# Kernel tuning notes

Hardware: AMD Instinct MI355X
Metric: run time of the kernel (lower is better)

The kernel has to match this reference:

```python
import jax, jax.numpy as jnp
import numpy as np

G, N, E, D, K = 32, 512, 8192, 256, 2048
LAMB_EDGE = 1.0
LAMB_NODE = 0.0
CODEBOOK_WEIGHT = 1000.0
ALPHA = 100.0


def setup_inputs() -> dict:
    key = jax.random.key(0)
    ks = jax.random.split(key, 12)
    s = 1.0 / np.sqrt(D)
    return {
        'feats': jax.random.normal(ks[0], (G, N, D), jnp.float32),
        'src': jax.random.randint(ks[1], (G, E), 0, N, jnp.int32),
        'dst': jax.random.randint(ks[2], (G, E), 0, N, jnp.int32),
        'W1': jax.random.normal(ks[3], (D, D), jnp.float32) * s,
        'b1': jnp.zeros((D,), jnp.float32),
        'W2': jax.random.normal(ks[4], (D, D), jnp.float32) * s,
        'b2': jnp.zeros((D,), jnp.float32),
        'ln_gamma': jnp.ones((D,), jnp.float32),
        'ln_beta': jnp.zeros((D,), jnp.float32),
        'dec1_W': jax.random.normal(ks[5], (D, D), jnp.float32) * s,
        'dec1_b': jnp.zeros((D,), jnp.float32),
        'dec2_W': jax.random.normal(ks[6], (D, D), jnp.float32) * s,
        'dec2_b': jnp.zeros((D,), jnp.float32),
        'codebook': jax.random.normal(ks[7], (K, D), jnp.float32),
    }


def _graph_conv(x, src, dst, W, b):
    # DGL GraphConv, norm='both': D_out^{-1/2} -> sum aggregate -> D_in^{-1/2} -> linear -> relu
    ones_e = jnp.ones(src.shape[0], x.dtype)
    deg_out = jnp.clip(jax.ops.segment_sum(ones_e, src, num_segments=N), 1.0)
    deg_in = jnp.clip(jax.ops.segment_sum(ones_e, dst, num_segments=N), 1.0)
    h = x * jax.lax.rsqrt(deg_out)[:, None]
    m = jax.ops.segment_sum(h[src], dst, num_segments=N)
    m = m * jax.lax.rsqrt(deg_in)[:, None]
    return jax.nn.relu(m @ W + b)


def _layernorm(x, gamma, beta):
    mu = jnp.mean(x, axis=-1, keepdims=True)
    var = jnp.mean(jnp.square(x - mu), axis=-1, keepdims=True)
    return (x - mu) * jax.lax.rsqrt(var + 1e-5) * gamma + beta


def _edge_loss(qe, src, dst):
    # qe: [N, D] decoded node embeddings for one graph
    logits = qe @ qe.T  # [N, N]
    adj = jnp.zeros((N, N), qe.dtype).at[src, dst].set(1.0)
    mask = jnp.triu(jnp.ones((N, N), bool), k=1)
    num_possible = N * N / 2.0
    num_edges = jnp.sum(jnp.where(mask, adj, 0.0))
    pos_weight = (num_possible - num_edges) / (num_edges + 1e-6)
    # BCEWithLogits with pos_weight, mean over strict upper triangle
    per = pos_weight * adj * jax.nn.softplus(-logits) + (1.0 - adj) * jax.nn.softplus(logits)
    return jnp.sum(jnp.where(mask, per, 0.0)) / (N * (N - 1) / 2.0)


def reference(feats, src, dst, W1, b1, W2, b2, ln_gamma, ln_beta,
              dec1_W, dec1_b, dec2_W, dec2_b, codebook):
    conv = jax.vmap(_graph_conv, in_axes=(0, 0, 0, None, None))
    h1 = conv(feats, src, dst, W1, b1)              # [G, N, D]
    h1 = _layernorm(h1, ln_gamma, ln_beta)           # dropout eval = identity
    h2 = conv(h1, src, dst, W2, b2)                  # [G, N, D]

    hf = h2.reshape(G * N, D)
    # cosine-sim VQ
    xn = hf * jax.lax.rsqrt(jnp.sum(hf * hf, -1, keepdims=True) + 1e-12)
    cn = codebook * jax.lax.rsqrt(jnp.sum(codebook * codebook, -1, keepdims=True) + 1e-12)
    dist = xn @ cn.T                                 # [G*N, K] cosine similarities
    idx = jnp.argmax(dist, axis=-1)
    q = codebook[idx]
    q_st = hf + jax.lax.stop_gradient(q - hf)        # straight-through
    vq_loss = CODEBOOK_WEIGHT * jnp.mean(jnp.square(q - jax.lax.stop_gradient(hf)))

    quantized_edge = (q_st @ dec1_W + dec1_b).reshape(G, N, D)
    quantized_node = q_st @ dec2_W + dec2_b

    edge_losses = jax.vmap(_edge_loss)(quantized_edge, src, dst)  # [G]
    edge_rec_loss = LAMB_EDGE * jnp.mean(edge_losses)
    feature_rec_loss = LAMB_NODE * jnp.mean(jnp.square(hf - quantized_node))
    loss = feature_rec_loss + edge_rec_loss * ALPHA + vq_loss
    return loss
```

## Files before the change

### kernel.cpp

```cpp
#include <hip/hip_runtime.h>
#include <math.h>

#define G 32
#define N 512
#define E 8192
#define D 256
#define KCB 2048
#define GN (G * N)

typedef __bf16 bf16x8 __attribute__((ext_vector_type(8)));
typedef float f32x4 __attribute__((ext_vector_type(4)));

static const size_t OFF_SPOS   = 0;
static const size_t OFF_SNEG   = OFF_SPOS + 256;
static const size_t OFF_BEST   = OFF_SNEG + 256;
static const size_t ZERO_BYTES = OFF_BEST + (size_t)GN * 8;
static const size_t OFF_NEDGE  = ZERO_BYTES;
static const size_t OFF_VQPART = OFF_NEDGE + 256;
static const size_t OFF_ROWOFF = OFF_VQPART + (size_t)GN * 4;
static const size_t OFF_RS_OUT = OFF_ROWOFF + (size_t)GN * 4;
static const size_t OFF_RS_IN  = OFF_RS_OUT + (size_t)GN * 4;
static const size_t OFF_DEG_IN = OFF_RS_IN + (size_t)GN * 4;
static const size_t OFF_CSR    = OFF_DEG_IN + (size_t)GN * 4;
static const size_t OFF_ADJ    = OFF_CSR + (size_t)G * E * 4;
static const size_t OFF_RNC    = OFF_ADJ + (size_t)G * N * N / 8;
static const size_t OFF_W1T    = OFF_RNC + (size_t)KCB * 4;
static const size_t OFF_W2T    = OFF_W1T + (size_t)D * D * 2;
static const size_t OFF_DWT    = OFF_W2T + (size_t)D * D * 2;
static const size_t OFF_CBB    = OFF_DWT + (size_t)D * D * 2;
static const size_t OFF_FEB    = OFF_CBB + (size_t)KCB * D * 2;
static const size_t OFF_AGGB   = OFF_FEB + (size_t)GN * D * 2;
static const size_t OFF_BF32   = OFF_AGGB + (size_t)GN * D * 2;
static const size_t OFF_BCB    = OFF_BF32 + (size_t)GN * D * 4;

__global__ void __launch_bounds__(512) k_graph_build(
    const int* __restrict__ src, const int* __restrict__ dst,
    unsigned* __restrict__ adj, int* __restrict__ nedge, int* __restrict__ row_off_g,
    float* __restrict__ rs_in_g, float* __restrict__ rs_out_g,
    int* __restrict__ deg_in_g, int* __restrict__ csr_src) {
  int g = blockIdx.x, t = threadIdx.x;
  __shared__ unsigned s_adj[N * N / 32];
  __shared__ int s_deg_in[N], s_deg_out[N];
  __shared__ int s_buf[2][N];
  __shared__ int s_red[8];
  for (int i = t; i < N * N / 32; i += 512) s_adj[i] = 0;
  s_deg_in[t] = 0;
  s_deg_out[t] = 0;
  __syncthreads();
  const int* sg = src + g * E;
  const int* dg = dst + g * E;
  int se[E / 512], de[E / 512];
  int ecount = 0;
#pragma unroll
  for (int j = 0; j < E / 512; ++j) {
    int s = sg[t + j * 512], d = dg[t + j * 512];
    se[j] = s; de[j] = d;
    atomicAdd(&s_deg_out[s], 1);
    atomicAdd(&s_deg_in[d], 1);
    if (s < d) {
      int bit = s * N + d;
      unsigned m = 1u << (bit & 31);
      unsigned old = atomicOr(&s_adj[bit >> 5], m);
      if (!(old & m)) ++ecount;
    }
  }
  __syncthreads();
  for (int off = 32; off; off >>= 1) ecount += __shfl_down(ecount, off);
  if ((t & 63) == 0) s_red[t >> 6] = ecount;
  __syncthreads();
  if (t == 0) {
    int tot = 0;
    for (int i = 0; i < 8; ++i) tot += s_red[i];
    nedge[g] = tot;
  }
  unsigned* adjg = adj + (size_t)g * (N * N / 32);
  for (int i = t; i < N * N / 32; i += 512) adjg[i] = s_adj[i];
  int own = s_deg_in[t];
  s_buf[0][t] = own;
  __syncthreads();
  int cur = 0;
  for (int off = 1; off < N; off <<= 1) {
    int v = s_buf[cur][t];
    if (t >= off) v += s_buf[cur][t - off];
    s_buf[cur ^ 1][t] = v;
    __syncthreads();
    cur ^= 1;
  }
  int roff = s_buf[cur][t] - own;
  row_off_g[g * N + t] = roff;
  deg_in_g[g * N + t] = own;
  rs_in_g[g * N + t] = rsqrtf(fmaxf((float)own, 1.0f));
  rs_out_g[g * N + t] = rsqrtf(fmaxf((float)s_deg_out[t], 1.0f));
  __syncthreads();
  s_deg_in[t] = roff;
  __syncthreads();
  int* csrg = csr_src + g * E;
#pragma unroll
  for (int j = 0; j < E / 512; ++j) {
    int slot = atomicAdd(&s_deg_in[de[j]], 1);
    csrg[slot] = se[j];
  }
}

__global__ void __launch_bounds__(256) k_prep(
    const float* __restrict__ W1, const float* __restrict__ W2,
    const float* __restrict__ dW, __bf16* __restrict__ W1t,
    __bf16* __restrict__ W2t, __bf16* __restrict__ dWt,
    const float* __restrict__ cb, __bf16* __restrict__ cbb, float* __restrict__ rnc) {
  int b = blockIdx.x;
  if (b < 192) {
    __shared__ float tile[32][33];
    int z = b / 64, tt = b % 64;
    int bx = (tt & 7) * 32, by = (tt >> 3) * 32;
    const float* in = z == 0 ? W1 : (z == 1 ? W2 : dW);
    __bf16* out = z == 0 ? W1t : (z == 1 ? W2t : dWt);
    int tx = threadIdx.x & 31, ty = threadIdx.x >> 5;
#pragma unroll
    for (int r = 0; r < 32; r += 8) tile[ty + r][tx] = in[(by + ty + r) * D + bx + tx];
    __syncthreads();
#pragma unroll
    for (int r = 0; r < 32; r += 8)
      out[(size_t)(bx + ty + r) * D + by + tx] = (__bf16)tile[tx][ty + r];
  } else {
    int row = b - 192, t = threadIdx.x;
    float v = cb[(size_t)row * D + t];
    cbb[(size_t)row * D + t] = (__bf16)v;
    float s2 = v * v;
    for (int off = 32; off; off >>= 1) s2 += __shfl_down(s2, off);
    __shared__ float w[4];
    if ((t & 63) == 0) w[t >> 6] = s2;
    __syncthreads();
    if (t == 0) rnc[row] = rsqrtf(w[0] + w[1] + w[2] + w[3] + 1e-12f);
  }
}

__global__ void k_cast_feats(const float* __restrict__ x, unsigned* __restrict__ xb2) {
  int i = blockIdx.x * 256 + threadIdx.x;
  float2 v = ((const float2*)x)[i];
  union { __bf16 h[2]; unsigned u; } o;
  o.h[0] = (__bf16)v.x; o.h[1] = (__bf16)v.y;
  xb2[i] = o.u;
}

__global__ void __launch_bounds__(128) k_aggregate(
    const unsigned* __restrict__ x2, const int* __restrict__ csr_src,
    const int* __restrict__ row_off, const int* __restrict__ deg_in,
    const float* __restrict__ rs_in, const float* __restrict__ rs_out,
    unsigned* __restrict__ out2) {
  int b = blockIdx.x;
  int g = ((b & 7) << 2) | (b >> 12);
  int n = (b >> 3) & 511;
  int gn = (g << 9) | n;
  int t = threadIdx.x;
  int cnt = deg_in[gn];
  int base = g * E + row_off[gn];
  __shared__ int sidx[128];
  __shared__ float sw[128];
  float ax = 0.f, ay = 0.f;
  for (int c0 = 0; c0 < cnt; c0 += 128) {
    int m = min(128, cnt - c0);
    if (t < m) {
      int s = csr_src[base + c0 + t];
      sidx[t] = s;
      sw[t] = rs_out[(g << 9) | s];
    }
    __syncthreads();
    for (int j = 0; j < m; ++j) {
      int s = sidx[j];
      float w = sw[j];
      unsigned v = x2[((size_t)((g << 9) | s) << 7) + t];
      ax += __uint_as_float(v << 16) * w;
      ay += __uint_as_float(v & 0xffff0000u) * w;
    }
    __syncthreads();
  }
  float ri = rs_in[gn];
  union { __bf16 h[2]; unsigned u; } o;
  o.h[0] = (__bf16)(ax * ri);
  o.h[1] = (__bf16)(ay * ri);
  out2[((size_t)gn << 7) + t] = o.u;
}

__device__ __forceinline__ void gload_lds16(const __bf16* g, __bf16* s) {
  __builtin_amdgcn_global_load_lds((const __attribute__((address_space(1))) void*)g,
                                   (__attribute__((address_space(3))) void*)s, 16, 0, 0);
}

__device__ __forceinline__ void mfma_core(const __bf16* __restrict__ Abase,
                                          const __bf16* __restrict__ Bbase,
                                          __bf16* sA, __bf16* sB, f32x4 (&acc)[4][4],
                                          int tid) {
  int wave = tid >> 6, lane = tid & 63;
  int wr = (wave >> 1) * 64, wc = (wave & 1) * 64;
  int m = lane & 15, quad = lane >> 4;
  for (int k0 = 0; k0 < 256; k0 += 32) {
#pragma unroll
    for (int c2 = 0; c2 < 2; ++c2) {
      int c = wave * 2 + c2;
      int row = c * 16 + (lane >> 2);
      int col = (lane & 3) * 8;
      gload_lds16(Abase + (size_t)row * 256 + k0 + col, sA + c * 512);
      gload_lds16(Bbase + (size_t)row * 256 + k0 + col, sB + c * 512);
    }
    __syncthreads();
    bf16x8 af[4], bfr[4];
#pragma unroll
    for (int i = 0; i < 4; ++i) {
      af[i] = *(const bf16x8*)&sA[(wr + i * 16 + m) * 32 + quad * 8];
      bfr[i] = *(const bf16x8*)&sB[(wc + i * 16 + m) * 32 + quad * 8];
    }
#pragma unroll
    for (int i = 0; i < 4; ++i)
#pragma unroll
      for (int j = 0; j < 4; ++j)
        acc[i][j] = __builtin_amdgcn_mfma_f32_16x16x32_bf16(af[i], bfr[j], acc[i][j], 0, 0, 0);
    __syncthreads();
  }
}

template <bool RELU, bool SF32, bool SBF16>
__global__ void __launch_bounds__(256) k_gemm_bf16(
    const __bf16* __restrict__ A, const __bf16* __restrict__ Bt,
    const float* __restrict__ bias, float* __restrict__ C, __bf16* __restrict__ Cb) {
  __shared__ __align__(16) __bf16 sA[4096], sB[4096];
  f32x4 acc[4][4] = {};
  int tid = threadIdx.x;
  int row0 = blockIdx.x * 128, col0 = blockIdx.y * 128;
  mfma_core(A + (size_t)row0 * 256, Bt + (size_t)col0 * 256, sA, sB, acc, tid);
  int wave = tid >> 6, lane = tid & 63;
  int wr = (wave >> 1) * 64, wc = (wave & 1) * 64, quad = lane >> 4, n16 = lane & 15;
#pragma unroll
  for (int j = 0; j < 4; ++j) {
    int col = col0 + wc + j * 16 + n16;
    float bs = bias[col];
#pragma unroll
    for (int i = 0; i < 4; ++i)
#pragma unroll
      for (int r = 0; r < 4; ++r) {
        int row = row0 + wr + i * 16 + quad * 4 + r;
        float v = acc[i][j][r] + bs;
        if (RELU) v = fmaxf(v, 0.f);
        if (SF32) C[(size_t)row * 256 + col] = v;
        if (SBF16) Cb[(size_t)row * 256 + col] = (__bf16)v;
      }
  }
}

__global__ void __launch_bounds__(128) k_layernorm(
    unsigned* __restrict__ xb2, const float* __restrict__ gamma,
    const float* __restrict__ beta) {
  int row = blockIdx.x, t = threadIdx.x;
  unsigned u = xb2[row * 128 + t];
  float vx = __uint_as_float(u << 16), vy = __uint_as_float(u & 0xffff0000u);
  float s = vx + vy, s2 = vx * vx + vy * vy;
  for (int off = 32; off; off >>= 1) {
    s += __shfl_down(s, off);
    s2 += __shfl_down(s2, off);
  }
  __shared__ float w1[2], w2[2];
  if ((t & 63) == 0) { w1[t >> 6] = s; w2[t >> 6] = s2; }
  __syncthreads();
  float mu = (w1[0] + w1[1]) * (1.f / D);
  float m2 = (w2[0] + w2[1]) * (1.f / D);
  float rstd = rsqrtf(m2 - mu * mu + 1e-5f);
  float2 gm = ((const float2*)gamma)[t];
  float2 bt = ((const float2*)beta)[t];
  union { __bf16 h[2]; unsigned u; } o;
  o.h[0] = (__bf16)((vx - mu) * rstd * gm.x + bt.x);
  o.h[1] = (__bf16)((vy - mu) * rstd * gm.y + bt.y);
  xb2[row * 128 + t] = o.u;
}

__global__ void __launch_bounds__(256) k_vq_bf16(
    const __bf16* __restrict__ A, const __bf16* __restrict__ CBt,
    const float* __restrict__ rnc, unsigned long long* __restrict__ best) {
  __shared__ __align__(16) __bf16 sA[4096], sB[4096];
  f32x4 acc[4][4] = {};
  int tid = threadIdx.x;
  int row0 = blockIdx.x * 128, col0 = blockIdx.y * 128;
  mfma_core(A + (size_t)row0 * 256, CBt + (size_t)col0 * 256, sA, sB, acc, tid);
  int wave = tid >> 6, lane = tid & 63;
  int wr = (wave >> 1) * 64, wc = (wave & 1) * 64, quad = lane >> 4, n16 = lane & 15;
#pragma unroll
  for (int i = 0; i < 4; ++i) {
    unsigned long long cand[4] = {0ull, 0ull, 0ull, 0ull};
#pragma unroll
    for (int j = 0; j < 4; ++j) {
      int col = col0 + wc + j * 16 + n16;
      float rc = rnc[col];
#pragma unroll
      for (int r = 0; r < 4; ++r) {
        float sim = acc[i][j][r] * rc;
        unsigned u = __float_as_uint(sim);
        u = ((int)u >= 0) ? (u | 0x80000000u) : ~u;
        unsigned long long c64 =
            ((unsigned long long)u << 32) | (0xFFFFFFFFu - (unsigned)col);
        cand[r] = cand[r] > c64 ? cand[r] : c64;
      }
    }
#pragma unroll
    for (int off = 1; off < 16; off <<= 1)
#pragma unroll
      for (int r = 0; r < 4; ++r) {
        unsigned long long o = __shfl_xor(cand[r], off, 64);
        cand[r] = cand[r] > o ? cand[r] : o;
      }
    if (n16 == 0)
#pragma unroll
      for (int r = 0; r < 4; ++r)
        atomicMax(&best[row0 + wr + i * 16 + quad * 4 + r], cand[r]);
  }
}

__global__ void k_vq_gather(const unsigned long long* __restrict__ best,
                            const float* __restrict__ cb, const __bf16* __restrict__ cbb,
                            const float* __restrict__ hf, __bf16* __restrict__ qb,
                            float* __restrict__ vq_part) {
  int row = blockIdx.x, t = threadIdx.x;
  unsigned long long b = best[row];
  int c = (int)(0xFFFFFFFFu - (unsigned)(b & 0xFFFFFFFFull));
  qb[(size_t)row * D + t] = cbb[(size_t)c * D + t];
  float d = cb[(size_t)c * D + t] - hf[(size_t)row * D + t];
  float s2 = d * d;
  for (int off = 32; off; off >>= 1) s2 += __shfl_down(s2, off);
  __shared__ float w[4];
  if ((t & 63) == 0) w[t >> 6] = s2;
  __syncthreads();
  if (t == 0) vq_part[row] = w[0] + w[1] + w[2] + w[3];
}

__constant__ int c_ti[10] = {0, 0, 0, 0, 1, 1, 1, 2, 2, 3};
__constant__ int c_tj[10] = {0, 1, 2, 3, 1, 2, 3, 2, 3, 3};

__global__ void __launch_bounds__(256) k_edge_bf16(
    const __bf16* __restrict__ qe, const unsigned* __restrict__ adj,
    float* __restrict__ Spos, float* __restrict__ Sneg) {
  int g = blockIdx.x / 10, p = blockIdx.x % 10;
  int row0 = c_ti[p] * 128, col0 = c_tj[p] * 128;
  const __bf16* Ag = qe + (size_t)g * N * D;
  const unsigned* adjg = adj + (size_t)g * (N * N / 32);
  __shared__ __align__(16) __bf16 sA[4096], sB[4096];
  f32x4 acc[4][4] = {};
  int tid = threadIdx.x;
  mfma_core(Ag + (size_t)row0 * 256, Ag + (size_t)col0 * 256, sA, sB, acc, tid);
  int wave = tid >> 6, lane = tid & 63;
  int wr = (wave >> 1) * 64, wc = (wave & 1) * 64, quad = lane >> 4, n16 = lane & 15;
  float spos = 0.f, sneg = 0.f;
#pragma unroll
  for (int i = 0; i < 4; ++i)
#pragma unroll
    for (int j = 0; j < 4; ++j) {
      int c = col0 + wc + j * 16 + n16;
#pragma unroll
      for (int r = 0; r < 4; ++r) {
        int rr = row0 + wr + i * 16 + quad * 4 + r;
        if (rr < c) {
          float l = acc[i][j][r];
          int bit = rr * N + c;
          bool a = (adjg[bit >> 5] >> (bit & 31)) & 1u;
          float spabs = log1pf(expf(-fabsf(l)));
          if (a) spos += fmaxf(-l, 0.f) + spabs;
          else sneg += fmaxf(l, 0.f) + spabs;
        }
      }
    }
  for (int off = 32; off; off >>= 1) {
    spos += __shfl_down(spos, off);
    sneg += __shfl_down(sneg, off);
  }
  __shared__ float wp[4], wn[4];
  if ((tid & 63) == 0) { wp[tid >> 6] = spos; wn[tid >> 6] = sneg; }
  __syncthreads();
  if (tid == 0) {
    atomicAdd(&Spos[g], wp[0] + wp[1] + wp[2] + wp[3]);
    atomicAdd(&Sneg[g], wn[0] + wn[1] + wn[2] + wn[3]);
  }
}

__global__ void __launch_bounds__(256) k_final(
    const int* __restrict__ nedge, const float* __restrict__ Spos,
    const float* __restrict__ Sneg, const float* __restrict__ vq_part,
    float* __restrict__ out) {
  int t = threadIdx.x;
  float vq = 0.f;
  for (int i = t; i < GN; i += 256) vq += vq_part[i];
  float el = 0.f;
  if (t < G) {
    float ne = (float)nedge[t];
    float pw = (131072.0f - ne) / (ne + 1e-6f);
    el = (pw * Spos[t] + Sneg[t]) * (1.0f / 130816.0f);
  }
  for (int off = 32; off; off >>= 1) {
    vq += __shfl_down(vq, off);
    el += __shfl_down(el, off);
  }
  __shared__ float wv[4], we[4];
  if ((t & 63) == 0) { wv[t >> 6] = vq; we[t >> 6] = el; }
  __syncthreads();
  if (t == 0) {
    float vqs = wv[0] + wv[1] + wv[2] + wv[3];
    float els = we[0] + we[1] + we[2] + we[3];
    out[0] = 100.0f * (els * (1.0f / G)) + 1000.0f * (vqs * (1.0f / ((float)GN * D)));
  }
}

extern "C" void kernel_launch(void* const* d_in, const int* in_sizes, int n_in,
                              void* d_out, int out_size, void* d_ws, size_t ws_size,
                              hipStream_t stream) {
  const float* feats = (const float*)d_in[0];
  const int* src = (const int*)d_in[1];
  const int* dst = (const int*)d_in[2];
  const float* W1 = (const float*)d_in[3];
  const float* b1 = (const float*)d_in[4];
  const float* W2 = (const float*)d_in[5];
  const float* b2 = (const float*)d_in[6];
  const float* ln_g = (const float*)d_in[7];
  const float* ln_b = (const float*)d_in[8];
  const float* dec1_W = (const float*)d_in[9];
  const float* dec1_b = (const float*)d_in[10];
  const float* cb = (const float*)d_in[13];

  char* ws = (char*)d_ws;
  float* Spos = (float*)(ws + OFF_SPOS);
  float* Sneg = (float*)(ws + OFF_SNEG);
  unsigned long long* best = (unsigned long long*)(ws + OFF_BEST);
  int* nedge = (int*)(ws + OFF_NEDGE);
  float* vq_part = (float*)(ws + OFF_VQPART);
  int* row_off = (int*)(ws + OFF_ROWOFF);
  float* rs_out = (float*)(ws + OFF_RS_OUT);
  float* rs_in = (float*)(ws + OFF_RS_IN);
  int* deg_in = (int*)(ws + OFF_DEG_IN);
  int* csr_src = (int*)(ws + OFF_CSR);
  unsigned* adj = (unsigned*)(ws + OFF_ADJ);
  float* rnc = (float*)(ws + OFF_RNC);
  __bf16* W1t = (__bf16*)(ws + OFF_W1T);
  __bf16* W2t = (__bf16*)(ws + OFF_W2T);
  __bf16* dWt = (__bf16*)(ws + OFF_DWT);
  __bf16* cbb = (__bf16*)(ws + OFF_CBB);
  unsigned* featsb2 = (unsigned*)(ws + OFF_FEB);
  __bf16* aggb = (__bf16*)(ws + OFF_AGGB);
  unsigned* aggb2 = (unsigned*)(ws + OFF_AGGB);
  float* bf32 = (float*)(ws + OFF_BF32);
  __bf16* bcb = (__bf16*)(ws + OFF_BCB);
  unsigned* bcb2 = (unsigned*)(ws + OFF_BCB);

  hipMemsetAsync(d_ws, 0, ZERO_BYTES, stream);

  k_graph_build<<<G, 512, 0, stream>>>(src, dst, adj, nedge, row_off, rs_in, rs_out,
                                       deg_in, csr_src);
  k_prep<<<192 + KCB, 256, 0, stream>>>(W1, W2, dec1_W, W1t, W2t, dWt, cb, cbb, rnc);
  k_cast_feats<<<GN * D / 512, 256, 0, stream>>>(feats, featsb2);

  k_aggregate<<<GN, 128, 0, stream>>>(featsb2, csr_src, row_off, deg_in, rs_in, rs_out,
                                      aggb2);
  k_gemm_bf16<true, false, true><<<dim3(GN / 128, 2), 256, 0, stream>>>(
      aggb, W1t, b1, nullptr, bcb);
  k_layernorm<<<GN, 128, 0, stream>>>(bcb2, ln_g, ln_b);

  k_aggregate<<<GN, 128, 0, stream>>>(bcb2, csr_src, row_off, deg_in, rs_in, rs_out, aggb2);
  k_gemm_bf16<true, true, true><<<dim3(GN / 128, 2), 256, 0, stream>>>(
      aggb, W2t, b2, bf32, bcb);

  k_vq_bf16<<<dim3(GN / 128, KCB / 128), 256, 0, stream>>>(bcb, cbb, rnc, best);
  k_vq_gather<<<GN, 256, 0, stream>>>(best, cb, cbb, bf32, bcb, vq_part);

  k_gemm_bf16<false, false, true><<<dim3(GN / 128, 2), 256, 0, stream>>>(
      bcb, dWt, dec1_b, nullptr, aggb);
  k_edge_bf16<<<10 * G, 256, 0, stream>>>(aggb, adj, Spos, Sneg);

  k_final<<<1, 256, 0, stream>>>(nedge, Spos, Sneg, vq_part, (float*)d_out);
}
```

Baseline: 275.0 us.

## Merge setup kernels into one launch and gather codebook rows inside decoder GEMM

Three preprocessing kernels (graph build, weight transpose/codebook cast, feature cast) are merged into a single launch that dispatches on block index. The per-row quantized-vector copy to a bf16 buffer is removed, and the decoder GEMM now loads codebook rows directly by argmax index into LDS. This cuts launch overhead and one full GN×D write/read round trip, at the cost of a large shared-memory footprint on every setup block and a gather-based A-tile load.

Result: faster. 267.1 us (median of 2 runs) (-2.8%).

```diff
diff --git a/kernel.cpp b/kernel.cpp
--- a/kernel.cpp
+++ b/kernel.cpp
@@ -33,113 +33,119 @@
 static const size_t OFF_BF32   = OFF_AGGB + (size_t)GN * D * 2;
 static const size_t OFF_BCB    = OFF_BF32 + (size_t)GN * D * 4;
 
-__global__ void __launch_bounds__(512) k_graph_build(
+__global__ void __launch_bounds__(512) k_setup(
     const int* __restrict__ src, const int* __restrict__ dst,
     unsigned* __restrict__ adj, int* __restrict__ nedge, int* __restrict__ row_off_g,
     float* __restrict__ rs_in_g, float* __restrict__ rs_out_g,
-    int* __restrict__ deg_in_g, int* __restrict__ csr_src) {
-  int g = blockIdx.x, t = threadIdx.x;
-  __shared__ unsigned s_adj[N * N / 32];
-  __shared__ int s_deg_in[N], s_deg_out[N];
-  __shared__ int s_buf[2][N];
-  __shared__ int s_red[8];
-  for (int i = t; i < N * N / 32; i += 512) s_adj[i] = 0;
-  s_deg_in[t] = 0;
-  s_deg_out[t] = 0;
-  __syncthreads();
-  const int* sg = src + g * E;
-  const int* dg = dst + g * E;
-  int se[E / 512], de[E / 512];
-  int ecount = 0;
-#pragma unroll
-  for (int j = 0; j < E / 512; ++j) {
-    int s = sg[t + j * 512], d = dg[t + j * 512];
-    se[j] = s; de[j] = d;
-    atomicAdd(&s_deg_out[s], 1);
-    atomicAdd(&s_deg_in[d], 1);
-    if (s < d) {
-      int bit = s * N + d;
-      unsigned m = 1u << (bit & 31);
-      unsigned old = atomicOr(&s_adj[bit >> 5], m);
-      if (!(old & m)) ++ecount;
-    }
-  }
-  __syncthreads();
-  for (int off = 32; off; off >>= 1) ecount += __shfl_down(ecount, off);
-  if ((t & 63) == 0) s_red[t >> 6] = ecount;
-  __syncthreads();
-  if (t == 0) {
-    int tot = 0;
-    for (int i = 0; i < 8; ++i) tot += s_red[i];
-    nedge[g] = tot;
-  }
-  unsigned* adjg = adj + (size_t)g * (N * N / 32);
-  for (int i = t; i < N * N / 32; i += 512) adjg[i] = s_adj[i];
-  int own = s_deg_in[t];
-  s_buf[0][t] = own;
-  __syncthreads();
-  int cur = 0;
-  for (int off = 1; off < N; off <<= 1) {
-    int v = s_buf[cur][t];
-    if (t >= off) v += s_buf[cur][t - off];
-    s_buf[cur ^ 1][t] = v;
-    __syncthreads();
-    cur ^= 1;
-  }
-  int roff = s_buf[cur][t] - own;
-  row_off_g[g * N + t] = roff;
-  deg_in_g[g * N + t] = own;
-  rs_in_g[g * N + t] = rsqrtf(fmaxf((float)own, 1.0f));
-  rs_out_g[g * N + t] = rsqrtf(fmaxf((float)s_deg_out[t], 1.0f));
-  __syncthreads();
-  s_deg_in[t] = roff;
-  __syncthreads();
-  int* csrg = csr_src + g * E;
-#pragma unroll
-  for (int j = 0; j < E / 512; ++j) {
-    int slot = atomicAdd(&s_deg_in[de[j]], 1);
-    csrg[slot] = se[j];
-  }
-}
-
-__global__ void __launch_bounds__(256) k_prep(
+    int* __restrict__ deg_in_g, int* __restrict__ csr_src,
     const float* __restrict__ W1, const float* __restrict__ W2,
     const float* __restrict__ dW, __bf16* __restrict__ W1t,
     __bf16* __restrict__ W2t, __bf16* __restrict__ dWt,
-    const float* __restrict__ cb, __bf16* __restrict__ cbb, float* __restrict__ rnc) {
-  int b = blockIdx.x;
-  if (b < 192) {
-    __shared__ float tile[32][33];
-    int z = b / 64, tt = b % 64;
+    const float* __restrict__ cb, __bf16* __restrict__ cbb, float* __restrict__ rnc,
+    const float* __restrict__ feats, unsigned* __restrict__ featsb2) {
+  __shared__ __align__(16) char smem[41088];
+  int b = blockIdx.x, t = threadIdx.x;
+  if (b < 32) {
+    int g = b;
+    unsigned* s_adj = (unsigned*)smem;
+    int* s_deg_in = (int*)(smem + 32768);
+    int* s_deg_out = (int*)(smem + 34816);
+    int(*s_buf)[N] = (int(*)[N])(smem + 36864);
+    int* s_red = (int*)(smem + 40960);
+    for (int i = t; i < N * N / 32; i += 512) s_adj[i] = 0;
+    s_deg_in[t] = 0;
+    s_deg_out[t] = 0;
+    __syncthreads();
+    const int* sg = src + g * E;
+    const int* dg = dst + g * E;
+    int se[E / 512], de[E / 512];
+    int ecount = 0;
+#pragma unroll
+    for (int j = 0; j < E / 512; ++j) {
+      int s = sg[t + j * 512], d = dg[t + j * 512];
+      se[j] = s; de[j] = d;
+      atomicAdd(&s_deg_out[s], 1);
+      atomicAdd(&s_deg_in[d], 1);
+      if (s < d) {
+        int bit = s * N + d;
+        unsigned m = 1u << (bit & 31);
+        unsigned old = atomicOr(&s_adj[bit >> 5], m);
+        if (!(old & m)) ++ecount;
+      }
+    }
+    __syncthreads();
+    for (int off = 32; off; off >>= 1) ecount += __shfl_down(ecount, off);
+    if ((t & 63) == 0) s_red[t >> 6] = ecount;
+    __syncthreads();
+    if (t == 0) {
+      int tot = 0;
+      for (int i = 0; i < 8; ++i) tot += s_red[i];
+      nedge[g] = tot;
+    }
+    unsigned* adjg = adj + (size_t)g * (N * N / 32);
+    for (int i = t; i < N * N / 32; i += 512) adjg[i] = s_adj[i];
+    int own = s_deg_in[t];
+    s_buf[0][t] = own;
+    __syncthreads();
+    int cur = 0;
+    for (int off = 1; off < N; off <<= 1) {
+      int v = s_buf[cur][t];
+      if (t >= off) v += s_buf[cur][t - off];
+      s_buf[cur ^ 1][t] = v;
+      __syncthreads();
+      cur ^= 1;
+    }
+    int roff = s_buf[cur][t] - own;
+    row_off_g[g * N + t] = roff;
+    deg_in_g[g * N + t] = own;
+    rs_in_g[g * N + t] = rsqrtf(fmaxf((float)own, 1.0f));
+    rs_out_g[g * N + t] = rsqrtf(fmaxf((float)s_deg_out[t], 1.0f));
+    __syncthreads();
+    s_deg_in[t] = roff;
+    __syncthreads();
+    int* csrg = csr_src + g * E;
+#pragma unroll
+    for (int j = 0; j < E / 512; ++j) {
+      int slot = atomicAdd(&s_deg_in[de[j]], 1);
+      csrg[slot] = se[j];
+    }
+  } else if (b < 224) {
+    float(*tile)[33] = (float(*)[33])smem;
+    int z = (b - 32) / 64, tt = (b - 32) % 64;
     int bx = (tt & 7) * 32, by = (tt >> 3) * 32;
     const float* in = z == 0 ? W1 : (z == 1 ? W2 : dW);
     __bf16* out = z == 0 ? W1t : (z == 1 ? W2t : dWt);
-    int tx = threadIdx.x & 31, ty = threadIdx.x >> 5;
-#pragma unroll
-    for (int r = 0; r < 32; r += 8) tile[ty + r][tx] = in[(by + ty + r) * D + bx + tx];
-    __syncthreads();
-#pragma unroll
-    for (int r = 0; r < 32; r += 8)
+    int tx = t & 31, ty = t >> 5;
+#pragma unroll
+    for (int r = 0; r < 32; r += 16) tile[ty + r][tx] = in[(by + ty + r) * D + bx + tx];
+    __syncthreads();
+#pragma unroll
+    for (int r = 0; r < 32; r += 16)
       out[(size_t)(bx + ty + r) * D + by + tx] = (__bf16)tile[tx][ty + r];
-  } else {
-    int row = b - 192, t = threadIdx.x;
-    float v = cb[(size_t)row * D + t];
-    cbb[(size_t)row * D + t] = (__bf16)v;
+  } else if (b < 1248) {
+    float* w = (float*)smem;
+    int row = (b - 224) * 2 + (t >> 8);
+    int col = t & 255;
+    float v = cb[(size_t)row * D + col];
+    cbb[(size_t)row * D + col] = (__bf16)v;
     float s2 = v * v;
     for (int off = 32; off; off >>= 1) s2 += __shfl_down(s2, off);
-    __shared__ float w[4];
     if ((t & 63) == 0) w[t >> 6] = s2;
     __syncthreads();
     if (t == 0) rnc[row] = rsqrtf(w[0] + w[1] + w[2] + w[3] + 1e-12f);
-  }
-}
-
-__global__ void k_cast_feats(const float* __restrict__ x, unsigned* __restrict__ xb2) {
-  int i = blockIdx.x * 256 + threadIdx.x;
-  float2 v = ((const float2*)x)[i];
-  union { __bf16 h[2]; unsigned u; } o;
-  o.h[0] = (__bf16)v.x; o.h[1] = (__bf16)v.y;
-  xb2[i] = o.u;
+    if (t == 256) rnc[row] = rsqrtf(w[4] + w[5] + w[6] + w[7] + 1e-12f);
+  } else {
+    int i0 = (b - 1248) * 2048 + t;
+#pragma unroll
+    for (int q = 0; q < 4; ++q) {
+      int i = i0 + q * 512;
+      float2 v = ((const float2*)feats)[i];
+      union { __bf16 h[2]; unsigned u; } o;
+      o.h[0] = (__bf16)v.x;
+      o.h[1] = (__bf16)v.y;
+      featsb2[i] = o.u;
+    }
+  }
 }
 
 __global__ void __launch_bounds__(128) k_aggregate(
@@ -246,6 +252,57 @@
   }
 }
 
+__global__ void __launch_bounds__(256) k_gemm_dec1(
+    const __bf16* __restrict__ cbb, const unsigned long long* __restrict__ best,
+    const __bf16* __restrict__ Bt, const float* __restrict__ bias,
+    __bf16* __restrict__ Cb) {
+  __shared__ __align__(16) __bf16 sA[4096], sB[4096];
+  f32x4 acc[4][4] = {};
+  int tid = threadIdx.x, wave = tid >> 6, lane = tid & 63;
+  int row0 = blockIdx.x * 128, col0 = blockIdx.y * 128;
+  int wr = (wave >> 1) * 64, wc = (wave & 1) * 64;
+  int m = lane & 15, quad = lane >> 4;
+  int c0 = wave * 2, c1 = wave * 2 + 1;
+  int idx0 = (int)(0xFFFFFFFFu -
+                   (unsigned)(best[row0 + c0 * 16 + (lane >> 2)] & 0xFFFFFFFFull));
+  int idx1 = (int)(0xFFFFFFFFu -
+                   (unsigned)(best[row0 + c1 * 16 + (lane >> 2)] & 0xFFFFFFFFull));
+  const __bf16* Bbase = Bt + (size_t)col0 * 256;
+  for (int k0 = 0; k0 < 256; k0 += 32) {
+    int col = (lane & 3) * 8;
+    gload_lds16(cbb + (size_t)idx0 * 256 + k0 + col, sA + c0 * 512);
+    gload_lds16(cbb + (size_t)idx1 * 256 + k0 + col, sA + c1 * 512);
+    gload_lds16(Bbase + (size_t)(c0 * 16 + (lane >> 2)) * 256 + k0 + col, sB + c0 * 512);
+    gload_lds16(Bbase + (size_t)(c1 * 16 + (lane >> 2)) * 256 + k0 + col, sB + c1 * 512);
+    __syncthreads();
+    bf16x8 af[4], bfr[4];
+#pragma unroll
+    for (int i = 0; i < 4; ++i) {
+      af[i] = *(const bf16x8*)&sA[(wr + i * 16 + m) * 32 + quad * 8];
+      bfr[i] = *(const bf16x8*)&sB[(wc + i * 16 + m) * 32 + quad * 8];
+    }
+#pragma unroll
+    for (int i = 0; i < 4; ++i)
+#pragma unroll
+      for (int j = 0; j < 4; ++j)
+        acc[i][j] = __builtin_amdgcn_mfma_f32_16x16x32_bf16(af[i], bfr[j], acc[i][j], 0, 0, 0);
+    __syncthreads();
+  }
+  int n16 = lane & 15;
+#pragma unroll
+  for (int j = 0; j < 4; ++j) {
+    int col = col0 + wc + j * 16 + n16;
+    float bs = bias[col];
+#pragma unroll
+    for (int i = 0; i < 4; ++i)
+#pragma unroll
+      for (int r = 0; r < 4; ++r) {
+        int row = row0 + wr + i * 16 + quad * 4 + r;
+        Cb[(size_t)row * 256 + col] = (__bf16)(acc[i][j][r] + bs);
+      }
+  }
+}
+
 __global__ void __launch_bounds__(128) k_layernorm(
     unsigned* __restrict__ xb2, const float* __restrict__ gamma,
     const float* __restrict__ beta) {
@@ -312,14 +369,12 @@
   }
 }
 
-__global__ void k_vq_gather(const unsigned long long* __restrict__ best,
-                            const float* __restrict__ cb, const __bf16* __restrict__ cbb,
-                            const float* __restrict__ hf, __bf16* __restrict__ qb,
-                            float* __restrict__ vq_part) {
+__global__ void k_vq_err(const unsigned long long* __restrict__ best,
+                         const float* __restrict__ cb, const float* __restrict__ hf,
+                         float* __restrict__ vq_part) {
   int row = blockIdx.x, t = threadIdx.x;
   unsigned long long b = best[row];
   int c = (int)(0xFFFFFFFFu - (unsigned)(b & 0xFFFFFFFFull));
-  qb[(size_t)row * D + t] = cbb[(size_t)c * D + t];
   float d = cb[(size_t)c * D + t] - hf[(size_t)row * D + t];
   float s2 = d * d;
   for (int off = 32; off; off >>= 1) s2 += __shfl_down(s2, off);
@@ -446,10 +501,9 @@
 
   hipMemsetAsync(d_ws, 0, ZERO_BYTES, stream);
 
-  k_graph_build<<<G, 512, 0, stream>>>(src, dst, adj, nedge, row_off, rs_in, rs_out,
-                                       deg_in, csr_src);
-  k_prep<<<192 + KCB, 256, 0, stream>>>(W1, W2, dec1_W, W1t, W2t, dWt, cb, cbb, rnc);
-  k_cast_feats<<<GN * D / 512, 256, 0, stream>>>(feats, featsb2);
+  k_setup<<<2272, 512, 0, stream>>>(src, dst, adj, nedge, row_off, rs_in, rs_out,
+                                    deg_in, csr_src, W1, W2, dec1_W, W1t, W2t, dWt,
+                                    cb, cbb, rnc, feats, featsb2);
 
   k_aggregate<<<GN, 128, 0, stream>>>(featsb2, csr_src, row_off, deg_in, rs_in, rs_out,
                                       aggb2);
@@ -462,10 +516,8 @@
       aggb, W2t, b2, bf32, bcb);
 
   k_vq_bf16<<<dim3(GN / 128, KCB / 128), 256, 0, stream>>>(bcb, cbb, rnc, best);
-  k_vq_gather<<<GN, 256, 0, stream>>>(best, cb, cbb, bf32, bcb, vq_part);
-
-  k_gemm_bf16<false, false, true><<<dim3(GN / 128, 2), 256, 0, stream>>>(
-      bcb, dWt, dec1_b, nullptr, aggb);
+  k_vq_err<<<GN, 256, 0, stream>>>(best, cb, bf32, vq_part);
+  k_gemm_dec1<<<dim3(GN / 128, 2), 256, 0, stream>>>(cbb, best, dWt, dec1_b, aggb);
   k_edge_bf16<<<10 * G, 256, 0, stream>>>(aggb, adj, Spos, Sneg);
 
   k_final<<<1, 256, 0, stream>>>(nedge, Spos, Sneg, vq_part, (float*)d_out);
```
